# Kernel tuning notes

Measured on AMD Instinct MI355X. Metric: run time of the kernel, lower is better.

## Reference

```python
import jax, jax.numpy as jnp
import numpy as np

B = 1024      # batch
HG = 28       # grid side (28x28 image -> graph)
N = HG * HG   # 784 nodes per sample
K = 70        # node_sampled (relaxed categorical classes)
GCN_OUT = 48
H_DIM = 400
Z = 70
IMG = 784
TEMP = 0.5


def _grid_edges():
    idx = np.arange(N).reshape(HG, HG)
    src = np.concatenate([idx[:, :-1].ravel(), idx[:, 1:].ravel(), idx[:-1, :].ravel(), idx[1:, :].ravel()])
    dst = np.concatenate([idx[:, 1:].ravel(), idx[:, :-1].ravel(), idx[1:, :].ravel(), idx[:-1, :].ravel()])
    loop = np.arange(N)
    return (np.concatenate([src, loop]).astype(np.int32),
            np.concatenate([dst, loop]).astype(np.int32))


def _lin(key, fi, fo):
    kw, kb = jax.random.split(key)
    s = 1.0 / np.sqrt(fi)
    return (jax.random.uniform(kw, (fi, fo), jnp.float32, -s, s),
            jax.random.uniform(kb, (fo,), jnp.float32, -s, s))


def setup_inputs() -> dict:
    key = jax.random.key(0)
    ks = jax.random.split(key, 16)
    src, dst = _grid_edges()
    u = jax.random.uniform(ks[2], (B, N, K), jnp.float32, 1e-6, 1.0 - 1e-6)
    inp = {
        'nodes': jax.random.normal(ks[0], (B, N, 2), jnp.float32),
        'logits': jax.random.normal(ks[1], (B, N, K), jnp.float32),
        'gumbel': -jnp.log(-jnp.log(u)),
        'eps': jax.random.normal(ks[3], (B, Z), jnp.float32),
    }
    inp['W1'], inp['b1'] = _lin(ks[4], 2, 16)
    inp['W2'], inp['b2'] = _lin(ks[5], 16, 32)
    inp['W3'], inp['b3'] = _lin(ks[6], 32, GCN_OUT)
    inp['We1'], inp['be1'] = _lin(ks[7], K * GCN_OUT, H_DIM)
    inp['We2'], inp['be2'] = _lin(ks[8], H_DIM, H_DIM)
    inp['Wmu'], inp['bmu'] = _lin(ks[9], H_DIM, Z)
    inp['Wvar'], inp['bvar'] = _lin(ks[10], H_DIM, Z)
    inp['Wd1'], inp['bd1'] = _lin(ks[11], Z, H_DIM)
    inp['Wd2'], inp['bd2'] = _lin(ks[12], H_DIM, IMG)
    inp['edge_src'] = jnp.asarray(src)
    inp['edge_dst'] = jnp.asarray(dst)
    return inp


def reference(nodes, logits, gumbel, eps,
              W1, b1, W2, b2, W3, b3,
              We1, be1, We2, be2,
              Wmu, bmu, Wvar, bvar,
              Wd1, bd1, Wd2, bd2,
              edge_src, edge_dst):
    # symmetric GCN normalization with self loops (already in edge list)
    deg = jnp.zeros((N,), nodes.dtype).at[edge_dst].add(1.0)
    dinv = jax.lax.rsqrt(deg)
    norm = dinv[edge_src] * dinv[edge_dst]  # [E]

    def gcn(h, W, b):
        h = h @ W                                   # [B,N,Fout]
        msg = h[:, edge_src] * norm[None, :, None]  # gather + scale, [B,E,Fout]
        return jnp.zeros_like(h).at[:, edge_dst].add(msg) + b

    h = jax.nn.relu(gcn(nodes, W1, b1))
    h = jax.nn.relu(gcn(h, W2, b2))
    h = jax.nn.relu(gcn(h, W3, b3))            # [B,N,48]

    # RelaxedOneHotCategorical(temp=0.5).rsample() == gumbel-softmax
    sample = jax.nn.softmax((logits + gumbel) / TEMP, axis=-1)  # [B,N,K]
    g = jnp.einsum('bnk,bnf->bkf', sample, h).reshape(h.shape[0], K * GCN_OUT)

    # encoder MLP + reparameterize
    e = jax.nn.relu(g @ We1 + be1)
    e = jax.nn.relu(e @ We2 + be2)
    mu = e @ Wmu + bmu
    var = jax.nn.softplus(e @ Wvar + bvar)
    z = mu + eps * jnp.sqrt(var + 1e-10)

    # decoder
    d = jax.nn.relu(z @ Wd1 + bd1)
    x_rec = jax.nn.sigmoid(d @ Wd2 + bd2)      # [B,784]
    return x_rec
```

## Files before the change

kernel.cpp:

```cpp
#include <hip/hip_runtime.h>
#include <hip/hip_bf16.h>


#define BB 1024
#define HG 28
#define NN 784
#define KK 70
#define F3 48
#define HD 400
#define ZD 70
#define IMGD 784

typedef __hip_bfloat16 bf16;
typedef __attribute__((ext_vector_type(8))) short s8v;
typedef __attribute__((ext_vector_type(4))) float f32x4;

__device__ __forceinline__ float dinv_ij(int i, int j){
  int deg = 1 + (i>0) + (i<HG-1) + (j>0) + (j<HG-1);
  return rsqrtf((float)deg);
}

__device__ __forceinline__ unsigned pk2(float a, float b){
  union { bf16 h; unsigned short u; } ua, ub;
  ua.h = __float2bfloat16(a); ub.h = __float2bfloat16(b);
  return ((unsigned)ub.u << 16) | ua.u;
}

__device__ __forceinline__ short bfbits(float v){
  union { bf16 h; short s; } u; u.h = __float2bfloat16(v); return u.s;
}

__global__ __launch_bounds__(256, 2)
void gcn_fused(const float* __restrict__ nodes,
               const float* __restrict__ W1, const float* __restrict__ b1,
               const float* __restrict__ W2, const float* __restrict__ b2,
               const float* __restrict__ W3, const float* __restrict__ b3,
               bf16* __restrict__ h3){
  __shared__ __align__(16) char smem[73216];
  float* regA = (float*)smem;
  float* regB = (float*)(smem + 36288);
  float* wbuf = (float*)(smem + 64512);
  float* W1s = wbuf;          float* b1s = wbuf + 32;
  float* W2s = wbuf + 48;     float* b2s = wbuf + 560;
  float* W3s = wbuf + 592;    float* b3s = wbuf + 2128;

  int tid = threadIdx.x;
  if (tid < 32)  W1s[tid] = W1[tid];
  if (tid < 16)  b1s[tid] = b1[tid];
  for (int t = tid; t < 512;  t += 256) W2s[t] = W2[t];
  if (tid < 32)  b2s[tid] = b2[tid];
  for (int t = tid; t < 1536; t += 256) W3s[t] = W3[t];
  if (tid < 48)  b3s[tid] = b3[tid];

  int b = blockIdx.x >> 2, s = blockIdx.x & 3;
  int base3 = s*7;
  int base2 = base3 - 1;
  int base1 = base3 - 2;
  const float* nb = nodes + (size_t)b*NN*2;
  __syncthreads();

  {
    float* h1s = regA;
    for (int t = tid; t < 308; t += 256){
      int lr = t/28, j = t - lr*28;
      int r = base1 + lr;
      float o[16] __attribute__((aligned(16)));
      if (r < 0 || r >= HG){
        #pragma unroll
        for (int f=0; f<16; f++) o[f] = 0.f;
      } else {
        float dn = dinv_ij(r,j);
        float a0 = dn*nb[(r*HG+j)*2+0], a1 = dn*nb[(r*HG+j)*2+1];
        if (r > 0)   { float w=dinv_ij(r-1,j); a0 += w*nb[((r-1)*HG+j)*2]; a1 += w*nb[((r-1)*HG+j)*2+1]; }
        if (r < HG-1){ float w=dinv_ij(r+1,j); a0 += w*nb[((r+1)*HG+j)*2]; a1 += w*nb[((r+1)*HG+j)*2+1]; }
        if (j > 0)   { float w=dinv_ij(r,j-1); a0 += w*nb[(r*HG+j-1)*2];   a1 += w*nb[(r*HG+j-1)*2+1]; }
        if (j < HG-1){ float w=dinv_ij(r,j+1); a0 += w*nb[(r*HG+j+1)*2];   a1 += w*nb[(r*HG+j+1)*2+1]; }
        a0 *= dn; a1 *= dn;
        #pragma unroll
        for (int f=0; f<16; f++) o[f] = fmaxf(a0*W1s[f] + a1*W1s[16+f] + b1s[f], 0.f);
      }
      float* dst = h1s + t*20;
      #pragma unroll
      for (int qq=0; qq<4; qq++) *(float4*)(dst + 4*qq) = *(float4*)&o[4*qq];
    }
  }
  __syncthreads();

  if (tid < 252){
    const float* h1s = regA;
    float* agg1 = regB;
    int lr = tid/28, j = tid - lr*28;
    int r = base2 + lr;
    float o[16] __attribute__((aligned(16)));
    if (r < 0 || r >= HG){
      #pragma unroll
      for (int f=0; f<16; f++) o[f] = 0.f;
    } else {
      int ln = (lr+1)*28 + j;
      float dn = dinv_ij(r,j);
      float wu = dinv_ij(r-1,j), wd = dinv_ij(r+1,j);
      float wl = (j>0)    ? dinv_ij(r,j-1) : 0.f;
      float wr = (j<HG-1) ? dinv_ij(r,j+1) : 0.f;
      const float* pc = h1s + ln*20;
      #pragma unroll
      for (int qq=0; qq<4; qq++){
        float4 vc = *(const float4*)(pc + 4*qq);
        float4 vu = *(const float4*)(pc - 28*20 + 4*qq);
        float4 vd = *(const float4*)(pc + 28*20 + 4*qq);
        float4 vl = *(const float4*)(pc - 20 + 4*qq);
        float4 vr = *(const float4*)(pc + 20 + 4*qq);
        o[4*qq+0] = dn*(dn*vc.x + wu*vu.x + wd*vd.x + wl*vl.x + wr*vr.x);
        o[4*qq+1] = dn*(dn*vc.y + wu*vu.y + wd*vd.y + wl*vl.y + wr*vr.y);
        o[4*qq+2] = dn*(dn*vc.z + wu*vu.z + wd*vd.z + wl*vl.z + wr*vr.z);
        o[4*qq+3] = dn*(dn*vc.w + wu*vu.w + wd*vd.w + wl*vl.w + wr*vr.w);
      }
    }
    float* dst = agg1 + tid*20;
    #pragma unroll
    for (int qq=0; qq<4; qq++) *(float4*)(dst + 4*qq) = *(float4*)&o[4*qq];
  }
  __syncthreads();

  {
    const float* agg1 = regB;
    float* h2s = regA;
    int tx = tid & 7, ty = tid >> 3;
    float4 w2r[16];
    #pragma unroll
    for (int fi=0; fi<16; fi++) w2r[fi] = *(const float4*)&W2s[fi*32 + tx*4];
    float4 bb = *(const float4*)&b2s[tx*4];
    #pragma unroll
    for (int i=0; i<8; i++){
      int n = ty + 32*i;
      if (n < 252){
        float af[16] __attribute__((aligned(16)));
        const float* ap = agg1 + n*20;
        #pragma unroll
        for (int qq=0; qq<4; qq++) *(float4*)&af[4*qq] = *(const float4*)(ap + 4*qq);
        float4 acc = bb;
        #pragma unroll
        for (int fi=0; fi<16; fi++){
          float a = af[fi];
          acc.x += a*w2r[fi].x; acc.y += a*w2r[fi].y;
          acc.z += a*w2r[fi].z; acc.w += a*w2r[fi].w;
        }
        acc.x = fmaxf(acc.x,0.f); acc.y = fmaxf(acc.y,0.f);
        acc.z = fmaxf(acc.z,0.f); acc.w = fmaxf(acc.w,0.f);
        *(float4*)&h2s[n*36 + tx*4] = acc;
      }
    }
  }
  __syncthreads();

  if (tid < 196){
    const float* h2s = regA;
    float* agg2 = regB;
    int lr = tid/28, j = tid - lr*28;
    int r = base3 + lr;
    int ln = (lr+1)*28 + j;
    float dn = dinv_ij(r,j);
    float wu = dinv_ij(r-1,j), wd = dinv_ij(r+1,j);
    float wl = (j>0)    ? dinv_ij(r,j-1) : 0.f;
    float wr = (j<HG-1) ? dinv_ij(r,j+1) : 0.f;
    const float* pc = h2s + ln*36;
    float* dst = agg2 + tid*36;
    #pragma unroll
    for (int qq=0; qq<8; qq++){
      float4 vc = *(const float4*)(pc + 4*qq);
      float4 vu = *(const float4*)(pc - 28*36 + 4*qq);
      float4 vd = *(const float4*)(pc + 28*36 + 4*qq);
      float4 vl = *(const float4*)(pc - 36 + 4*qq);
      float4 vr = *(const float4*)(pc + 36 + 4*qq);
      float4 o;
      o.x = dn*(dn*vc.x + wu*vu.x + wd*vd.x + wl*vl.x + wr*vr.x);
      o.y = dn*(dn*vc.y + wu*vu.y + wd*vd.y + wl*vl.y + wr*vr.y);
      o.z = dn*(dn*vc.z + wu*vu.z + wd*vd.z + wl*vl.z + wr*vr.z);
      o.w = dn*(dn*vc.w + wu*vu.w + wd*vd.w + wl*vl.w + wr*vr.w);
      *(float4*)(dst + 4*qq) = o;
    }
  }
  __syncthreads();

  {
    bf16* h3buf = (bf16*)regA;
    if (tid < 252){
      const float* agg2 = regB;
      int tx = tid % 12, ty = tid / 12;
      float4 w3r[32];
      #pragma unroll
      for (int fi=0; fi<32; fi++) w3r[fi] = *(const float4*)&W3s[fi*48 + tx*4];
      float4 bb = *(const float4*)&b3s[tx*4];
      #pragma unroll
      for (int i=0; i<10; i++){
        int n = ty + 21*i;
        if (n < 196){
          float af[32] __attribute__((aligned(16)));
          const float* ap = agg2 + n*36;
          #pragma unroll
          for (int qq=0; qq<8; qq++) *(float4*)&af[4*qq] = *(const float4*)(ap + 4*qq);
          float4 acc = bb;
          #pragma unroll
          for (int fi=0; fi<32; fi++){
            float a = af[fi];
            acc.x += a*w3r[fi].x; acc.y += a*w3r[fi].y;
            acc.z += a*w3r[fi].z; acc.w += a*w3r[fi].w;
          }
          uint2 pv;
          pv.x = pk2(fmaxf(acc.x,0.f), fmaxf(acc.y,0.f));
          pv.y = pk2(fmaxf(acc.z,0.f), fmaxf(acc.w,0.f));
          *(uint2*)((char*)h3buf + n*112 + tx*8) = pv;
        }
      }
    }
  }
  __syncthreads();

  {
    const char* h3buf = (const char*)regA;
    uint4* dst = (uint4*)(h3 + ((size_t)b*NN + base3*28)*F3);
    for (int t = tid; t < 1176; t += 256){
      int n = t/6, gq = t - n*6;
      dst[t] = *(const uint4*)(h3buf + n*112 + gq*16);
    }
  }
}

__global__ __launch_bounds__(256)
void einsum_mfma_kernel(const float* __restrict__ logits, const float* __restrict__ gumbel,
                        const bf16* __restrict__ h3, float* __restrict__ g){
  __shared__ __align__(16) unsigned smemD[2][7488];
  const int SLO = 2880, HTO = 5760;

  int b = blockIdx.x, tid = threadIdx.x;
  int l = tid & 63, w = tid >> 6;
  int n_loc = tid >> 2, q = tid & 3;
  int kstart = q << 4;
  int kcnt = (q < 3) ? 16 : 22;
  int kc2 = kcnt >> 1;
  int m_pair = tid >> 3;
  int half = (tid >> 2) & 1;
  int ks = w >> 1, mh = w & 1;
  int mtoff = mh ? 3 : 0, mtcnt = mh ? 2 : 3;

  for (int t = tid; t < 720; t += 256){
    int bb = t >= 360, r = t - bb*360;
    smemD[bb][2520 + r] = 0u;
    smemD[bb][SLO + 2520 + r] = 0u;
  }

  f32x4 acc[3][3];
  #pragma unroll
  for (int mt=0; mt<3; mt++)
    #pragma unroll
    for (int bt=0; bt<3; bt++) acc[mt][bt] = (f32x4){0.f,0.f,0.f,0.f};

  float2 lx[11], gx[11];
  uint2 hA0, hB0, hA1, hB1;
  int hm0 = tid/12, hj0 = tid - hm0*12;
  int tt1 = tid + 256;
  int hm1 = tt1/12, hj1 = tt1 - hm1*12;

  auto issue_loads = [&](int c){
    int c0 = c << 6;
    int node = c0 + n_loc;
    bool v = node < NN;
    const float* lp = logits + ((size_t)b*NN + node)*KK + kstart;
    const float* gp = gumbel + ((size_t)b*NN + node)*KK + kstart;
    int nld = (q < 3) ? 8 : 11;
    #pragma unroll
    for (int s=0; s<11; s++){
      bool a = v && (s < nld);
      lx[s] = a ? *(const float2*)(lp + 2*s) : (float2){0.f,0.f};
      gx[s] = a ? *(const float2*)(gp + 2*s) : (float2){0.f,0.f};
    }
    bool vA0 = (c0 + 2*hm0)     < NN;
    bool vB0 = (c0 + 2*hm0 + 1) < NN;
    const uint2* p0 = (const uint2*)(h3 + ((size_t)b*NN + c0 + 2*hm0)*F3 + 4*hj0);
    hA0 = vA0 ? p0[0]  : (uint2){0u,0u};
    hB0 = vB0 ? p0[12] : (uint2){0u,0u};
    if (tid < 128){
      bool vA1 = (c0 + 2*hm1)     < NN;
      bool vB1 = (c0 + 2*hm1 + 1) < NN;
      const uint2* p1 = (const uint2*)(h3 + ((size_t)b*NN + c0 + 2*hm1)*F3 + 4*hj1);
      hA1 = vA1 ? p1[0]  : (uint2){0u,0u};
      hB1 = vB1 ? p1[12] : (uint2){0u,0u};
    }
  };

  auto consume = [&](int c, unsigned* buf){
    int c0 = c << 6;
    bool v = (c0 + n_loc) < NN;
    float x[22];
    #pragma unroll
    for (int s=0; s<11; s++){
      x[2*s]   = 2.f*(lx[s].x + gx[s].x);
      x[2*s+1] = 2.f*(lx[s].y + gx[s].y);
    }
    float mx = -1e30f;
    #pragma unroll
    for (int i=0; i<22; i++) if (i < kcnt) mx = fmaxf(mx, x[i]);
    mx = fmaxf(mx, __shfl_xor(mx, 1));
    mx = fmaxf(mx, __shfl_xor(mx, 2));
    float sum = 0.f;
    #pragma unroll
    for (int i=0; i<22; i++) if (i < kcnt){ x[i] = __expf(x[i]-mx); sum += x[i]; }
    sum += __shfl_xor(sum, 1);
    sum += __shfl_xor(sum, 2);
    float rs = v ? 1.0f/sum : 0.f;
    #pragma unroll
    for (int i=0; i<22; i++){
      if (i < kcnt){
        float p = x[i]*rs;
        unsigned hb = (unsigned)(unsigned short)bfbits(p);
        union { short s; bf16 h; } uh; uh.s = (short)hb;
        float lo = p - __bfloat162float(uh.h);
        unsigned lb = (unsigned)(unsigned short)bfbits(lo);
        unsigned phb = (unsigned)__shfl_xor((int)hb, 4);
        unsigned plb = (unsigned)__shfl_xor((int)lb, 4);
        unsigned dh = (half==0) ? (hb | (phb<<16)) : (phb | (hb<<16));
        unsigned dl = (half==0) ? (lb | (plb<<16)) : (plb | (lb<<16));
        bool doW = (half==0) ? (i < kc2) : (i >= kc2);
        if (doW){
          int k = kstart + i;
          int col = m_pair ^ (((k>>4)&3)<<3);
          buf[k*36 + col] = dh;
          buf[SLO + k*36 + col] = dl;
        }
      }
    }
    {
      unsigned d0 = (hA0.x & 0xFFFFu) | (hB0.x << 16);
      unsigned d1 = (hA0.x >> 16)     | (hB0.x & 0xFFFF0000u);
      unsigned d2 = (hA0.y & 0xFFFFu) | (hB0.y << 16);
      unsigned d3 = (hA0.y >> 16)     | (hB0.y & 0xFFFF0000u);
      #pragma unroll
      for (int i2=0; i2<4; i2++){
        int f = 4*hj0 + i2;
        int col = hm0 ^ (((f>>4)&3)<<3);
        unsigned dv = (i2==0)?d0:(i2==1)?d1:(i2==2)?d2:d3;
        buf[HTO + f*36 + col] = dv;
      }
      if (tid < 128){
        unsigned e0 = (hA1.x & 0xFFFFu) | (hB1.x << 16);
        unsigned e1 = (hA1.x >> 16)     | (hB1.x & 0xFFFF0000u);
        unsigned e2 = (hA1.y & 0xFFFFu) | (hB1.y << 16);
        unsigned e3 = (hA1.y >> 16)     | (hB1.y & 0xFFFF0000u);
        #pragma unroll
        for (int i2=0; i2<4; i2++){
          int f = 4*hj1 + i2;
          int col = hm1 ^ (((f>>4)&3)<<3);
          unsigned dv = (i2==0)?e0:(i2==1)?e1:(i2==2)?e2:e3;
          buf[HTO + f*36 + col] = dv;
        }
      }
    }
  };

  auto mfma_phase = [&](const unsigned* buf){
    int pr = (ks<<4) + ((l>>4)<<2);
    s8v Af[3], Al[3], Bf[3];
    #pragma unroll
    for (int mt=0; mt<3; mt++) if (mt < mtcnt){
      int row = (mtoff+mt)*16 + (l&15);
      int col = pr ^ (((row>>4)&3)<<3);
      Af[mt] = *(const s8v*)&buf[row*36 + col];
      Al[mt] = *(const s8v*)&buf[SLO + row*36 + col];
    }
    #pragma unroll
    for (int bt=0; bt<3; bt++){
      int f = bt*16 + (l&15);
      int col = pr ^ (((f>>4)&3)<<3);
      Bf[bt] = *(const s8v*)&buf[HTO + f*36 + col];
    }
    #pragma unroll
    for (int mt=0; mt<3; mt++) if (mt < mtcnt)
      #pragma unroll
      for (int bt=0; bt<3; bt++){
        acc[mt][bt] = __builtin_amdgcn_mfma_f32_16x16x32_bf16(Af[mt], Bf[bt], acc[mt][bt], 0, 0, 0);
        acc[mt][bt] = __builtin_amdgcn_mfma_f32_16x16x32_bf16(Al[mt], Bf[bt], acc[mt][bt], 0, 0, 0);
      }
  };

  issue_loads(0);
  consume(0, smemD[0]);
  issue_loads(1);
  __syncthreads();
  for (int c = 0; c < 13; c++){
    if (c < 12){
      consume(c+1, smemD[(c+1)&1]);
      if (c + 2 <= 12) issue_loads(c+2);
    }
    mfma_phase(smemD[c&1]);
    __syncthreads();
  }

  float* cred = (float*)&smemD[0][0];
  if (ks == 0){
    #pragma unroll
    for (int mt=0; mt<3; mt++) if (mt < mtcnt)
      #pragma unroll
      for (int bt=0; bt<3; bt++)
        #pragma unroll
        for (int r=0; r<4; r++){
          int row = (mtoff+mt)*16 + (l>>4)*4 + r;
          int col = bt*16 + (l&15);
          cred[row*49 + col] = acc[mt][bt][r];
        }
  }
  __syncthreads();
  if (ks == 1){
    #pragma unroll
    for (int mt=0; mt<3; mt++) if (mt < mtcnt)
      #pragma unroll
      for (int bt=0; bt<3; bt++)
        #pragma unroll
        for (int r=0; r<4; r++){
          int row = (mtoff+mt)*16 + (l>>4)*4 + r;
          int col = bt*16 + (l&15);
          cred[row*49 + col] += acc[mt][bt][r];
        }
  }
  __syncthreads();
  for (int t = tid; t < KK*F3; t += 256){
    int r = t / F3, c2 = t - r*F3;
    g[(size_t)b*(KK*F3) + t] = cred[r*49 + c2];
  }
}

template<int ACT>
__global__ __launch_bounds__(256)
void dense_kernel(const float* __restrict__ A, const float* __restrict__ W,
                  const float* __restrict__ bias, float* __restrict__ out,
                  int M, int K, int Nn, int kChunk){
  __shared__ float As[16][65];
  __shared__ float Bs[16][64];
  int tx = threadIdx.x & 15, ty = threadIdx.x >> 4;
  int m0 = blockIdx.x*64, n0 = blockIdx.y*64;
  int ks = blockIdx.z * kChunk;
  int ke = min(K, ks + kChunk);
  int a_kk = threadIdx.x & 15, a_mm = threadIdx.x >> 4;
  int b_nn = threadIdx.x & 63, b_k0 = threadIdx.x >> 6;
  float ra[4], rb[4];
  float acc[4][4] = {};

  #pragma unroll
  for (int s=0; s<4; s++){
    int gk = ks + a_kk;
    ra[s] = (gk < ke) ? A[(size_t)(m0 + a_mm + s*16)*K + gk] : 0.f;
  }
  #pragma unroll
  for (int s=0; s<4; s++){
    int gk = ks + b_k0 + s*4, gn = n0 + b_nn;
    rb[s] = (gk < ke && gn < Nn) ? W[(size_t)gk*Nn + gn] : 0.f;
  }

  for (int k0 = ks; k0 < ke; k0 += 16){
    #pragma unroll
    for (int s=0; s<4; s++) As[a_kk][a_mm + s*16] = ra[s];
    #pragma unroll
    for (int s=0; s<4; s++) Bs[b_k0 + s*4][b_nn] = rb[s];
    __syncthreads();
    if (k0 + 16 < ke){
      #pragma unroll
      for (int s=0; s<4; s++){
        int gk = k0 + 16 + a_kk;
        ra[s] = (gk < ke) ? A[(size_t)(m0 + a_mm + s*16)*K + gk] : 0.f;
      }
      #pragma unroll
      for (int s=0; s<4; s++){
        int gk = k0 + 16 + b_k0 + s*4, gn = n0 + b_nn;
        rb[s] = (gk < ke && gn < Nn) ? W[(size_t)gk*Nn + gn] : 0.f;
      }
    }
    #pragma unroll
    for (int kk=0; kk<16; kk++){
      float a[4], bv[4];
      #pragma unroll
      for (int i2=0; i2<4; i2++) a[i2] = As[kk][ty*4+i2];
      #pragma unroll
      for (int j2=0; j2<4; j2++) bv[j2] = Bs[kk][tx*4+j2];
      #pragma unroll
      for (int i2=0; i2<4; i2++)
        #pragma unroll
        for (int j2=0; j2<4; j2++) acc[i2][j2] += a[i2]*bv[j2];
    }
    __syncthreads();
  }

  if (ACT == 2){
    float* po = out + (size_t)blockIdx.z*M*Nn;
    #pragma unroll
    for (int j2=0; j2<4; j2++){
      int gn = n0 + tx*4 + j2;
      if (gn < Nn){
        #pragma unroll
        for (int i2=0; i2<4; i2++)
          po[(size_t)(m0 + ty*4 + i2)*Nn + gn] = acc[i2][j2];
      }
    }
  } else {
    #pragma unroll
    for (int j2=0; j2<4; j2++){
      int gn = n0 + tx*4 + j2;
      if (gn < Nn){
        float bb = bias[gn];
        #pragma unroll
        for (int i2=0; i2<4; i2++){
          float v = acc[i2][j2] + bb;
          v = (ACT == 0) ? fmaxf(v, 0.f) : 1.0f/(1.0f + __expf(-v));
          out[(size_t)(m0 + ty*4 + i2)*Nn + gn] = v;
        }
      }
    }
  }
}

__global__ __launch_bounds__(256)
void reduce_bias_relu(const float* __restrict__ part, const float* __restrict__ bias,
                      float* __restrict__ out, int M, int Nn, int S){
  int idx = blockIdx.x*256 + threadIdx.x;
  if (idx >= M*Nn) return;
  int n = idx % Nn;
  float s = bias[n];
  for (int i=0; i<S; i++) s += part[(size_t)i*M*Nn + idx];
  out[idx] = fmaxf(s, 0.f);
}

__global__ __launch_bounds__(256)
void latent_kernel(const float* __restrict__ e2,
                   const float* __restrict__ Wmu, const float* __restrict__ bmu,
                   const float* __restrict__ Wvar, const float* __restrict__ bvar,
                   const float* __restrict__ eps, float* __restrict__ z){
  int idx = blockIdx.x*256 + threadIdx.x;
  int b = idx / ZD, zi = idx - b*ZD;
  const float* er = e2 + (size_t)b*HD;
  float amu = 0.f, avr = 0.f;
  for (int j=0; j<HD; j++){
    float e = er[j];
    amu += e*Wmu[j*ZD + zi];
    avr += e*Wvar[j*ZD + zi];
  }
  float mu = amu + bmu[zi];
  float va = avr + bvar[zi];
  float sp = fmaxf(va, 0.f) + log1pf(__expf(-fabsf(va)));
  z[idx] = mu + eps[idx]*sqrtf(sp + 1e-10f);
}

extern "C" void kernel_launch(void* const* d_in, const int* in_sizes, int n_in,
                              void* d_out, int out_size, void* d_ws, size_t ws_size,
                              hipStream_t stream){
  (void)in_sizes; (void)n_in; (void)out_size; (void)ws_size;
  const float* nodes  = (const float*)d_in[0];
  const float* logits = (const float*)d_in[1];
  const float* gumbel = (const float*)d_in[2];
  const float* eps    = (const float*)d_in[3];
  const float* W1 =(const float*)d_in[4],  *b1 =(const float*)d_in[5];
  const float* W2 =(const float*)d_in[6],  *b2 =(const float*)d_in[7];
  const float* W3 =(const float*)d_in[8],  *b3 =(const float*)d_in[9];
  const float* We1=(const float*)d_in[10], *be1=(const float*)d_in[11];
  const float* We2=(const float*)d_in[12], *be2=(const float*)d_in[13];
  const float* Wmu=(const float*)d_in[14], *bmu=(const float*)d_in[15];
  const float* Wvr=(const float*)d_in[16], *bvr=(const float*)d_in[17];
  const float* Wd1=(const float*)d_in[18], *bd1=(const float*)d_in[19];
  const float* Wd2=(const float*)d_in[20], *bd2=(const float*)d_in[21];

  char* ws = (char*)d_ws;
  bf16*  h3 = (bf16*)(ws);
  float* g  = (float*)(ws + 77070336);
  float* e1 = (float*)(ws + 90832896);
  float* e2 = (float*)(ws + 92471296);
  float* zb = (float*)(ws + 94109696);
  float* dd = (float*)(ws + 94396416);
  float* part = (float*)(ws);
  float* out = (float*)d_out;

  gcn_fused<<<4096, 256, 0, stream>>>(nodes, W1, b1, W2, b2, W3, b3, h3);
  einsum_mfma_kernel<<<1024, 256, 0, stream>>>(logits, gumbel, h3, g);
  dense_kernel<2><<<dim3(16, 7, 8), 256, 0, stream>>>(g, We1, nullptr, part, 1024, 3360, 400, 432);
  reduce_bias_relu<<<1600, 256, 0, stream>>>(part, be1, e1, 1024, 400, 8);
  dense_kernel<0><<<dim3(16, 7, 1), 256, 0, stream>>>(e1, We2, be2, e2, 1024, 400, 400, 400);
  latent_kernel<<<280, 256, 0, stream>>>(e2, Wmu, bmu, Wvr, bvr, eps, zb);
  dense_kernel<0><<<dim3(16, 7, 1), 256, 0, stream>>>(zb, Wd1, bd1, dd, 1024, 70, 400, 70);
  dense_kernel<1><<<dim3(16, 13, 1), 256, 0, stream>>>(dd, Wd2, bd2, out, 1024, 400, 784, 400);
}
```

Baseline: 422.1 us.

## Split-K the small dense layers, batch latent GEMM, and double-buffer einsum loads

Runs the e2, latent and final decoder GEMMs as split-K partial GEMMs followed by reduction kernels, so these small-grid launches fill more CUs. The latent projection becomes a tiled GEMM over a concatenated mu/var output instead of one thread per output looping over 400 inputs. The einsum kernel gets two register sets so global loads are issued two chunks ahead, and uses a barrier that waits only on LDS traffic. The GCN layer-3 loop is split in halves to lower register pressure. These add extra launches and partial-sum memory traffic in exchange.

```diff
diff --git a/kernel.cpp b/kernel.cpp
--- a/kernel.cpp
+++ b/kernel.cpp
@@ -29,6 +29,13 @@
 __device__ __forceinline__ short bfbits(float v){
   union { bf16 h; short s; } u; u.h = __float2bfloat16(v); return u.s;
 }
+
+#define SYNC_LDS() do {                                   \
+    asm volatile("" ::: "memory");                        \
+    asm volatile("s_waitcnt lgkmcnt(0)" ::: "memory");    \
+    __builtin_amdgcn_s_barrier();                         \
+    asm volatile("" ::: "memory");                        \
+  } while(0)
 
 __global__ __launch_bounds__(256, 2)
 void gcn_fused(const float* __restrict__ nodes,
@@ -186,28 +193,39 @@
     if (tid < 252){
       const float* agg2 = regB;
       int tx = tid % 12, ty = tid / 12;
-      float4 w3r[32];
-      #pragma unroll
-      for (int fi=0; fi<32; fi++) w3r[fi] = *(const float4*)&W3s[fi*48 + tx*4];
+      float4 accv[10];
       float4 bb = *(const float4*)&b3s[tx*4];
+      #pragma unroll
+      for (int i=0; i<10; i++) accv[i] = bb;
+      #pragma unroll
+      for (int hh=0; hh<2; hh++){
+        float4 w3r[16];
+        #pragma unroll
+        for (int fi=0; fi<16; fi++) w3r[fi] = *(const float4*)&W3s[(hh*16+fi)*48 + tx*4];
+        #pragma unroll
+        for (int i=0; i<10; i++){
+          int n = ty + 21*i;
+          if (n < 196){
+            const float* ap = agg2 + n*36 + hh*16;
+            float af[16] __attribute__((aligned(16)));
+            #pragma unroll
+            for (int qq=0; qq<4; qq++) *(float4*)&af[4*qq] = *(const float4*)(ap + 4*qq);
+            #pragma unroll
+            for (int fi=0; fi<16; fi++){
+              float a = af[fi];
+              accv[i].x += a*w3r[fi].x; accv[i].y += a*w3r[fi].y;
+              accv[i].z += a*w3r[fi].z; accv[i].w += a*w3r[fi].w;
+            }
+          }
+        }
+      }
       #pragma unroll
       for (int i=0; i<10; i++){
         int n = ty + 21*i;
         if (n < 196){
-          float af[32] __attribute__((aligned(16)));
-          const float* ap = agg2 + n*36;
-          #pragma unroll
-          for (int qq=0; qq<8; qq++) *(float4*)&af[4*qq] = *(const float4*)(ap + 4*qq);
-          float4 acc = bb;
-          #pragma unroll
-          for (int fi=0; fi<32; fi++){
-            float a = af[fi];
-            acc.x += a*w3r[fi].x; acc.y += a*w3r[fi].y;
-            acc.z += a*w3r[fi].z; acc.w += a*w3r[fi].w;
-          }
           uint2 pv;
-          pv.x = pk2(fmaxf(acc.x,0.f), fmaxf(acc.y,0.f));
-          pv.y = pk2(fmaxf(acc.z,0.f), fmaxf(acc.w,0.f));
+          pv.x = pk2(fmaxf(accv[i].x,0.f), fmaxf(accv[i].y,0.f));
+          pv.y = pk2(fmaxf(accv[i].z,0.f), fmaxf(accv[i].w,0.f));
           *(uint2*)((char*)h3buf + n*112 + tx*8) = pv;
         }
       }
@@ -254,13 +272,15 @@
     #pragma unroll
     for (int bt=0; bt<3; bt++) acc[mt][bt] = (f32x4){0.f,0.f,0.f,0.f};
 
-  float2 lx[11], gx[11];
-  uint2 hA0, hB0, hA1, hB1;
+  float2 lxA[11], gxA[11], lxB[11], gxB[11];
+  uint2 hA0A, hB0A, hA1A, hB1A;
+  uint2 hA0B, hB0B, hA1B, hB1B;
   int hm0 = tid/12, hj0 = tid - hm0*12;
   int tt1 = tid + 256;
   int hm1 = tt1/12, hj1 = tt1 - hm1*12;
 
-  auto issue_loads = [&](int c){
+  auto issue_into = [&](int c, float2 (&lx)[11], float2 (&gx)[11],
+                        uint2& hA0, uint2& hB0, uint2& hA1, uint2& hB1){
     int c0 = c << 6;
     int node = c0 + n_loc;
     bool v = node < NN;
@@ -287,7 +307,8 @@
     }
   };
 
-  auto consume = [&](int c, unsigned* buf){
+  auto consume_from = [&](int c, unsigned* buf, float2 (&lx)[11], float2 (&gx)[11],
+                          uint2& hA0, uint2& hB0, uint2& hA1, uint2& hB1){
     int c0 = c << 6;
     bool v = (c0 + n_loc) < NN;
     float x[22];
@@ -381,17 +402,22 @@
       }
   };
 
-  issue_loads(0);
-  consume(0, smemD[0]);
-  issue_loads(1);
-  __syncthreads();
+  issue_into(0, lxA, gxA, hA0A, hB0A, hA1A, hB1A);
+  issue_into(1, lxB, gxB, hA0B, hB0B, hA1B, hB1B);
+  consume_from(0, smemD[0], lxA, gxA, hA0A, hB0A, hA1A, hB1A);
+  SYNC_LDS();
+
   for (int c = 0; c < 13; c++){
+    if (c + 2 <= 12){
+      if ((c & 1) == 0) issue_into(c+2, lxA, gxA, hA0A, hB0A, hA1A, hB1A);
+      else              issue_into(c+2, lxB, gxB, hA0B, hB0B, hA1B, hB1B);
+    }
     if (c < 12){
-      consume(c+1, smemD[(c+1)&1]);
-      if (c + 2 <= 12) issue_loads(c+2);
+      if (((c+1) & 1) == 0) consume_from(c+1, smemD[(c+1)&1], lxA, gxA, hA0A, hB0A, hA1A, hB1A);
+      else                  consume_from(c+1, smemD[(c+1)&1], lxB, gxB, hA0B, hB0B, hA1B, hB1B);
     }
     mfma_phase(smemD[c&1]);
-    __syncthreads();
+    SYNC_LDS();
   }
 
   float* cred = (float*)&smemD[0][0];
@@ -516,32 +542,99 @@
 }
 
 __global__ __launch_bounds__(256)
-void reduce_bias_relu(const float* __restrict__ part, const float* __restrict__ bias,
-                      float* __restrict__ out, int M, int Nn, int S){
+void dense_dualB_partial(const float* __restrict__ A, const float* __restrict__ Wmu,
+                         const float* __restrict__ Wvar, float* __restrict__ out,
+                         int M, int K, int Nn, int kChunk){
+  __shared__ float As[16][65];
+  __shared__ float Bs[16][64];
+  int tx = threadIdx.x & 15, ty = threadIdx.x >> 4;
+  int m0 = blockIdx.x*64, n0 = blockIdx.y*64;
+  int ks = blockIdx.z * kChunk;
+  int ke = min(K, ks + kChunk);
+  int a_kk = threadIdx.x & 15, a_mm = threadIdx.x >> 4;
+  int b_nn = threadIdx.x & 63, b_k0 = threadIdx.x >> 6;
+  float ra[4], rb[4];
+  float acc[4][4] = {};
+
+  auto bload = [&](int gk, int gn)->float{
+    if (gk >= ke || gn >= Nn) return 0.f;
+    return (gn < ZD) ? Wmu[(size_t)gk*ZD + gn] : Wvar[(size_t)gk*ZD + gn - ZD];
+  };
+
+  #pragma unroll
+  for (int s=0; s<4; s++){
+    int gk = ks + a_kk;
+    ra[s] = (gk < ke) ? A[(size_t)(m0 + a_mm + s*16)*K + gk] : 0.f;
+  }
+  #pragma unroll
+  for (int s=0; s<4; s++) rb[s] = bload(ks + b_k0 + s*4, n0 + b_nn);
+
+  for (int k0 = ks; k0 < ke; k0 += 16){
+    #pragma unroll
+    for (int s=0; s<4; s++) As[a_kk][a_mm + s*16] = ra[s];
+    #pragma unroll
+    for (int s=0; s<4; s++) Bs[b_k0 + s*4][b_nn] = rb[s];
+    __syncthreads();
+    if (k0 + 16 < ke){
+      #pragma unroll
+      for (int s=0; s<4; s++){
+        int gk = k0 + 16 + a_kk;
+        ra[s] = (gk < ke) ? A[(size_t)(m0 + a_mm + s*16)*K + gk] : 0.f;
+      }
+      #pragma unroll
+      for (int s=0; s<4; s++) rb[s] = bload(k0 + 16 + b_k0 + s*4, n0 + b_nn);
+    }
+    #pragma unroll
+    for (int kk=0; kk<16; kk++){
+      float a[4], bv[4];
+      #pragma unroll
+      for (int i2=0; i2<4; i2++) a[i2] = As[kk][ty*4+i2];
+      #pragma unroll
+      for (int j2=0; j2<4; j2++) bv[j2] = Bs[kk][tx*4+j2];
+      #pragma unroll
+      for (int i2=0; i2<4; i2++)
+        #pragma unroll
+        for (int j2=0; j2<4; j2++) acc[i2][j2] += a[i2]*bv[j2];
+    }
+    __syncthreads();
+  }
+
+  float* po = out + (size_t)blockIdx.z*M*Nn;
+  #pragma unroll
+  for (int j2=0; j2<4; j2++){
+    int gn = n0 + tx*4 + j2;
+    if (gn < Nn){
+      #pragma unroll
+      for (int i2=0; i2<4; i2++)
+        po[(size_t)(m0 + ty*4 + i2)*Nn + gn] = acc[i2][j2];
+    }
+  }
+}
+
+template<int ACT>
+__global__ __launch_bounds__(256)
+void reduce_bias_act(const float* __restrict__ part, const float* __restrict__ bias,
+                     float* __restrict__ out, int M, int Nn, int S){
   int idx = blockIdx.x*256 + threadIdx.x;
   if (idx >= M*Nn) return;
   int n = idx % Nn;
   float s = bias[n];
   for (int i=0; i<S; i++) s += part[(size_t)i*M*Nn + idx];
-  out[idx] = fmaxf(s, 0.f);
+  out[idx] = (ACT == 0) ? fmaxf(s, 0.f) : 1.0f/(1.0f + __expf(-s));
 }
 
 __global__ __launch_bounds__(256)
-void latent_kernel(const float* __restrict__ e2,
-                   const float* __restrict__ Wmu, const float* __restrict__ bmu,
-                   const float* __restrict__ Wvar, const float* __restrict__ bvar,
-                   const float* __restrict__ eps, float* __restrict__ z){
+void reduce_reparam(const float* __restrict__ part, const float* __restrict__ bmu,
+                    const float* __restrict__ bvar, const float* __restrict__ eps,
+                    float* __restrict__ z, int S){
   int idx = blockIdx.x*256 + threadIdx.x;
   int b = idx / ZD, zi = idx - b*ZD;
-  const float* er = e2 + (size_t)b*HD;
-  float amu = 0.f, avr = 0.f;
-  for (int j=0; j<HD; j++){
-    float e = er[j];
-    amu += e*Wmu[j*ZD + zi];
-    avr += e*Wvar[j*ZD + zi];
-  }
-  float mu = amu + bmu[zi];
-  float va = avr + bvar[zi];
+  float mu = bmu[zi], va = bvar[zi];
+  for (int s=0; s<S; s++){
+    const float* pr = part + ((size_t)s*BB + b)*140;
+    mu += pr[zi];
+    va += pr[ZD + zi];
+  }
   float sp = fmaxf(va, 0.f) + log1pf(__expf(-fabsf(va)));
   z[idx] = mu + eps[idx]*sqrtf(sp + 1e-10f);
 }
@@ -577,9 +670,12 @@
   gcn_fused<<<4096, 256, 0, stream>>>(nodes, W1, b1, W2, b2, W3, b3, h3);
   einsum_mfma_kernel<<<1024, 256, 0, stream>>>(logits, gumbel, h3, g);
   dense_kernel<2><<<dim3(16, 7, 8), 256, 0, stream>>>(g, We1, nullptr, part, 1024, 3360, 400, 432);
-  reduce_bias_relu<<<1600, 256, 0, stream>>>(part, be1, e1, 1024, 400, 8);
-  dense_kernel<0><<<dim3(16, 7, 1), 256, 0, stream>>>(e1, We2, be2, e2, 1024, 400, 400, 400);
-  latent_kernel<<<280, 256, 0, stream>>>(e2, Wmu, bmu, Wvr, bvr, eps, zb);
+  reduce_bias_act<0><<<1600, 256, 0, stream>>>(part, be1, e1, 1024, 400, 8);
+  dense_kernel<2><<<dim3(16, 7, 4), 256, 0, stream>>>(e1, We2, nullptr, part, 1024, 400, 400, 112);
+  reduce_bias_act<0><<<1600, 256, 0, stream>>>(part, be2, e2, 1024, 400, 4);
+  dense_dualB_partial<<<dim3(16, 3, 4), 256, 0, stream>>>(e2, Wmu, Wvr, part, 1024, 400, 140, 112);
+  reduce_reparam<<<280, 256, 0, stream>>>(part, bmu, bvr, eps, zb, 4);
   dense_kernel<0><<<dim3(16, 7, 1), 256, 0, stream>>>(zb, Wd1, bd1, dd, 1024, 70, 400, 70);
-  dense_kernel<1><<<dim3(16, 13, 1), 256, 0, stream>>>(dd, Wd2, bd2, out, 1024, 400, 784, 400);
-}
+  dense_kernel<2><<<dim3(16, 13, 4), 256, 0, stream>>>(dd, Wd2, nullptr, part, 1024, 400, 784, 112);
+  reduce_bias_act<1><<<3136, 256, 0, stream>>>(part, bd2, out, 1024, 784, 4);
+}
```

After: 645.2 us. +52.8%, slower.
